# Kernel tuning notes

Hardware: AMD Instinct MI355X
Metric: run time of the kernel (lower is better)

Reference implementation:

```python
import jax, jax.numpy as jnp
import numpy as np

SIM_THRESHOLD = 0.65  # recall() returns decoded memory only if best_sim > 0.65
EPS = 1e-8            # torch F.cosine_similarity default eps


def setup_inputs() -> dict:
    key = jax.random.key(0)
    k1, k2, k3, k4 = jax.random.split(key, 4)
    dim, seq, n_mem = 1024, 2048, 131072
    bound = 1.0 / np.sqrt(dim)  # nn.Linear default init scale
    return {
        "query": jax.random.normal(k1, (seq, dim), dtype=jnp.float32),
        "bank": jax.random.normal(k2, (n_mem, dim), dtype=jnp.float32),
        "w_dec": jax.random.uniform(k3, (dim, dim), dtype=jnp.float32, minval=-bound, maxval=bound),
        "b_dec": jax.random.uniform(k4, (dim,), dtype=jnp.float32, minval=-bound, maxval=bound),
    }


def reference(query, bank, w_dec, b_dec):
    # q = query.detach().mean(dim=0)
    q = query.mean(axis=0)                                   # [dim]
    # cosine similarity of q against every stored memory (batched version of
    # the per-item F.cosine_similarity loop): dot / (max(||a||,eps)*max(||b||,eps))
    q_norm = jnp.maximum(jnp.linalg.norm(q), EPS)
    bank_norms = jnp.maximum(jnp.linalg.norm(bank, axis=1), EPS)  # [N]
    sims = (bank @ q) / (bank_norms * q_norm)                 # [N]
    idx = jnp.argmax(sims)
    best_sim = sims[idx]
    best_mem = bank[idx]                                      # [dim]
    # decoder(best.embedding): Linear(dim, dim)
    decoded = best_mem @ w_dec.T + b_dec                      # [dim]
    # original returns None below threshold; model as zeros to keep static shape
    return jnp.where(best_sim > SIM_THRESHOLD, decoded, jnp.zeros_like(decoded))
```

## Files before the change

### kernel.cpp

```cpp
#include <hip/hip_runtime.h>

#define EPS 1e-8f
#define THR 0.65f

constexpr int DIM  = 1024;
constexpr int SEQ  = 2048;
constexpr int NMEM = 131072;

constexpr int NCOPY    = 8;
constexpr int SIM_BLKS = 2048;
constexpr int ROWS_PER_WAVE = NMEM / (SIM_BLKS * 4);

typedef float f4 __attribute__((ext_vector_type(4)));

constexpr int WS_Q     = 8192;
constexpr int WS_QNORM = 9216;
constexpr int WS_BESTS = 9218;

__global__ void init_kernel(float* __restrict__ ws) {
    ((float4*)ws)[blockIdx.x * 256 + threadIdx.x] = make_float4(0.f, 0.f, 0.f, 0.f);
}

__global__ void qsum_kernel(const float* __restrict__ query, float* __restrict__ ws) {
    const float4* q4 = (const float4*)query;
    int tid = threadIdx.x;
    int r0  = blockIdx.x * 8;
    float4 s = make_float4(0.f, 0.f, 0.f, 0.f);
    #pragma unroll
    for (int r = 0; r < 8; ++r) {
        float4 v = q4[(size_t)(r0 + r) * 256 + tid];
        s.x += v.x; s.y += v.y; s.z += v.z; s.w += v.w;
    }
    float* dst = ws + (blockIdx.x & (NCOPY - 1)) * DIM + tid * 4;
    atomicAdd(dst + 0, s.x);
    atomicAdd(dst + 1, s.y);
    atomicAdd(dst + 2, s.z);
    atomicAdd(dst + 3, s.w);
}

__global__ void qfinal_kernel(float* __restrict__ ws) {
    __shared__ float red[4];
    int tid = threadIdx.x;
    float4 v = make_float4(0.f, 0.f, 0.f, 0.f);
    #pragma unroll
    for (int c = 0; c < NCOPY; ++c) {
        float4 p = ((float4*)ws)[c * 256 + tid];
        v.x += p.x; v.y += p.y; v.z += p.z; v.w += p.w;
    }
    const float inv = 1.0f / (float)SEQ;
    v.x *= inv; v.y *= inv; v.z *= inv; v.w *= inv;
    ((float4*)(ws + WS_Q))[tid] = v;
    float ss = v.x * v.x + v.y * v.y + v.z * v.z + v.w * v.w;
    #pragma unroll
    for (int m = 32; m >= 1; m >>= 1) ss += __shfl_xor(ss, m);
    int lane = tid & 63, wid = tid >> 6;
    if (lane == 0) red[wid] = ss;
    __syncthreads();
    if (tid == 0) {
        float tot = red[0] + red[1] + red[2] + red[3];
        ws[WS_QNORM] = fmaxf(sqrtf(tot), EPS);
    }
}

__device__ __forceinline__ unsigned int float_to_ordered(float f) {
    unsigned int b = __float_as_uint(f);
    return (b & 0x80000000u) ? ~b : (b | 0x80000000u);
}

__device__ __forceinline__ unsigned long long pack_best(float sim, int idx) {
    return ((unsigned long long)float_to_ordered(sim) << 32) |
           (unsigned int)(~(unsigned int)idx);
}

__launch_bounds__(256, 4)
__global__ void sim_kernel(const float* __restrict__ bank, const float* __restrict__ ws,
                           unsigned long long* __restrict__ bests) {
    __shared__ unsigned long long wbest[4];
    int tid  = threadIdx.x;
    int lane = tid & 63;
    int wid  = tid >> 6;

    const f4* q4 = (const f4*)(ws + WS_Q);
    f4 q0 = q4[lane +   0];
    f4 q1 = q4[lane +  64];
    f4 q2 = q4[lane + 128];
    f4 q3 = q4[lane + 192];
    float qn = ws[WS_QNORM];

    int gw   = blockIdx.x * 4 + wid;
    int row0 = gw * ROWS_PER_WAVE;

    float bestSim = -1e30f;
    int   bestIdx = 0;

    #pragma unroll
    for (int g = 0; g < ROWS_PER_WAVE / 4; ++g) {
        float dot[4], ss[4];
        f4 b[4][4];
        #pragma unroll
        for (int r = 0; r < 4; ++r) {
            const f4* bp = (const f4*)(bank + (size_t)(row0 + g * 4 + r) * DIM);
            b[r][0] = __builtin_nontemporal_load(bp + lane +   0);
            b[r][1] = __builtin_nontemporal_load(bp + lane +  64);
            b[r][2] = __builtin_nontemporal_load(bp + lane + 128);
            b[r][3] = __builtin_nontemporal_load(bp + lane + 192);
        }
        #pragma unroll
        for (int r = 0; r < 4; ++r) {
            dot[r] = b[r][0].x*q0.x + b[r][0].y*q0.y + b[r][0].z*q0.z + b[r][0].w*q0.w
                   + b[r][1].x*q1.x + b[r][1].y*q1.y + b[r][1].z*q1.z + b[r][1].w*q1.w
                   + b[r][2].x*q2.x + b[r][2].y*q2.y + b[r][2].z*q2.z + b[r][2].w*q2.w
                   + b[r][3].x*q3.x + b[r][3].y*q3.y + b[r][3].z*q3.z + b[r][3].w*q3.w;
            ss[r]  = b[r][0].x*b[r][0].x + b[r][0].y*b[r][0].y + b[r][0].z*b[r][0].z + b[r][0].w*b[r][0].w
                   + b[r][1].x*b[r][1].x + b[r][1].y*b[r][1].y + b[r][1].z*b[r][1].z + b[r][1].w*b[r][1].w
                   + b[r][2].x*b[r][2].x + b[r][2].y*b[r][2].y + b[r][2].z*b[r][2].z + b[r][2].w*b[r][2].w
                   + b[r][3].x*b[r][3].x + b[r][3].y*b[r][3].y + b[r][3].z*b[r][3].z + b[r][3].w*b[r][3].w;
        }
        #pragma unroll
        for (int m = 32; m >= 1; m >>= 1) {
            #pragma unroll
            for (int r = 0; r < 4; ++r) {
                dot[r] += __shfl_xor(dot[r], m);
                ss[r]  += __shfl_xor(ss[r], m);
            }
        }
        #pragma unroll
        for (int r = 0; r < 4; ++r) {
            float bn  = fmaxf(sqrtf(ss[r]), EPS);
            float sim = dot[r] / (bn * qn);
            if (sim > bestSim) { bestSim = sim; bestIdx = row0 + g * 4 + r; }
        }
    }

    if (lane == 0) wbest[wid] = pack_best(bestSim, bestIdx);
    __syncthreads();
    if (tid == 0) {
        unsigned long long p = wbest[0];
        if (wbest[1] > p) p = wbest[1];
        if (wbest[2] > p) p = wbest[2];
        if (wbest[3] > p) p = wbest[3];
        bests[blockIdx.x] = p;
    }
}

__global__ void decode_kernel(const float* __restrict__ bank,
                              const float* __restrict__ w_dec,
                              const float* __restrict__ b_dec,
                              const unsigned long long* __restrict__ bests,
                              float* __restrict__ out) {
    __shared__ unsigned long long red[256];
    __shared__ float mem[DIM];
    int tid = threadIdx.x;

    unsigned long long p = bests[tid];
    #pragma unroll
    for (int i = 1; i < SIM_BLKS / 256; ++i) {
        unsigned long long v = bests[tid + i * 256];
        if (v > p) p = v;
    }
    red[tid] = p;
    __syncthreads();
    #pragma unroll
    for (int s = 128; s >= 1; s >>= 1) {
        if (tid < s) {
            if (red[tid + s] > red[tid]) red[tid] = red[tid + s];
        }
        __syncthreads();
    }
    p = red[0];
    unsigned int u = (unsigned int)(p >> 32);
    unsigned int fb = (u & 0x80000000u) ? (u & 0x7FFFFFFFu) : ~u;
    float sim = __uint_as_float(fb);
    int idx   = (int)(~(unsigned int)(p & 0xFFFFFFFFu));

    ((float4*)mem)[tid] = ((const float4*)(bank + (size_t)idx * DIM))[tid];
    __syncthreads();

    bool ok  = sim > THR;
    int lane = tid & 63, wid = tid >> 6;
    int row  = blockIdx.x * 4 + wid;

    const float4* wp = (const float4*)(w_dec + (size_t)row * DIM);
    const float4* m4 = (const float4*)mem;
    float dot = 0.f;
    #pragma unroll
    for (int it = 0; it < 4; ++it) {
        float4 w = wp[lane + it * 64];
        float4 m = m4[lane + it * 64];
        dot += w.x * m.x + w.y * m.y + w.z * m.z + w.w * m.w;
    }
    #pragma unroll
    for (int m = 32; m >= 1; m >>= 1) dot += __shfl_xor(dot, m);

    if (lane == 0) out[row] = ok ? (dot + b_dec[row]) : 0.0f;
}

extern "C" void kernel_launch(void* const* d_in, const int* in_sizes, int n_in,
                              void* d_out, int out_size, void* d_ws, size_t ws_size,
                              hipStream_t stream) {
    const float* query = (const float*)d_in[0];
    const float* bank  = (const float*)d_in[1];
    const float* w_dec = (const float*)d_in[2];
    const float* b_dec = (const float*)d_in[3];
    float* out = (float*)d_out;
    float* ws  = (float*)d_ws;
    unsigned long long* bests = (unsigned long long*)(ws + WS_BESTS);

    init_kernel<<<NCOPY, 256, 0, stream>>>(ws);
    qsum_kernel<<<SEQ / 8, 256, 0, stream>>>(query, ws);
    qfinal_kernel<<<1, 256, 0, stream>>>(ws);
    sim_kernel<<<SIM_BLKS, 256, 0, stream>>>(bank, ws, bests);
    decode_kernel<<<256, 256, 0, stream>>>(bank, w_dec, b_dec, bests, out);
}
```

Baseline: 110.6 us.

## Replace atomic query-mean reduction with two-stage deterministic partial-sum kernels

The query column sum no longer uses float atomics into replicated buffers plus init and final kernels. A first kernel writes per-block partial sums to workspace, and a second kernel of 8 blocks reduces them, writing the mean and per-slice squared-norm partials. The sim kernel now combines those partials into the query norm itself. This removes one launch and the atomic contention, at the cost of an extra 1 MB of partial-sum traffic; the launch_bounds occupancy hint on sim_kernel is also relaxed.

```diff
diff --git a/kernel.cpp b/kernel.cpp
--- a/kernel.cpp
+++ b/kernel.cpp
@@ -7,58 +7,47 @@
 constexpr int SEQ  = 2048;
 constexpr int NMEM = 131072;
 
-constexpr int NCOPY    = 8;
 constexpr int SIM_BLKS = 2048;
 constexpr int ROWS_PER_WAVE = NMEM / (SIM_BLKS * 4);
 
 typedef float f4 __attribute__((ext_vector_type(4)));
 
-constexpr int WS_Q     = 8192;
-constexpr int WS_QNORM = 9216;
-constexpr int WS_BESTS = 9218;
-
-__global__ void init_kernel(float* __restrict__ ws) {
-    ((float4*)ws)[blockIdx.x * 256 + threadIdx.x] = make_float4(0.f, 0.f, 0.f, 0.f);
-}
-
-__global__ void qsum_kernel(const float* __restrict__ query, float* __restrict__ ws) {
-    const float4* q4 = (const float4*)query;
-    int tid = threadIdx.x;
-    int r0  = blockIdx.x * 8;
-    float4 s = make_float4(0.f, 0.f, 0.f, 0.f);
-    #pragma unroll
-    for (int r = 0; r < 8; ++r) {
-        float4 v = q4[(size_t)(r0 + r) * 256 + tid];
-        s.x += v.x; s.y += v.y; s.z += v.z; s.w += v.w;
-    }
-    float* dst = ws + (blockIdx.x & (NCOPY - 1)) * DIM + tid * 4;
-    atomicAdd(dst + 0, s.x);
-    atomicAdd(dst + 1, s.y);
-    atomicAdd(dst + 2, s.z);
-    atomicAdd(dst + 3, s.w);
-}
-
-__global__ void qfinal_kernel(float* __restrict__ ws) {
-    __shared__ float red[4];
-    int tid = threadIdx.x;
-    float4 v = make_float4(0.f, 0.f, 0.f, 0.f);
-    #pragma unroll
-    for (int c = 0; c < NCOPY; ++c) {
-        float4 p = ((float4*)ws)[c * 256 + tid];
-        v.x += p.x; v.y += p.y; v.z += p.z; v.w += p.w;
-    }
-    const float inv = 1.0f / (float)SEQ;
-    v.x *= inv; v.y *= inv; v.z *= inv; v.w *= inv;
-    ((float4*)(ws + WS_Q))[tid] = v;
-    float ss = v.x * v.x + v.y * v.y + v.z * v.z + v.w * v.w;
-    #pragma unroll
-    for (int m = 32; m >= 1; m >>= 1) ss += __shfl_xor(ss, m);
-    int lane = tid & 63, wid = tid >> 6;
-    if (lane == 0) red[wid] = ss;
-    __syncthreads();
-    if (tid == 0) {
-        float tot = red[0] + red[1] + red[2] + red[3];
-        ws[WS_QNORM] = fmaxf(sqrtf(tot), EPS);
+constexpr int WS_Q     = 262144;
+constexpr int WS_SSP   = 263168;
+constexpr int WS_BESTS = 263178;
+
+__global__ void qsumA_kernel(const float* __restrict__ query, float* __restrict__ ws) {
+    int t = threadIdx.x;
+    int b = blockIdx.x;
+    const f4* qp = (const f4*)(query + (size_t)b * 8 * DIM) + t;
+    f4 s = qp[0];
+    #pragma unroll
+    for (int r = 1; r < 8; ++r) s += qp[r * 256];
+    ((f4*)ws)[b * 256 + t] = s;
+}
+
+__global__ void qsumB_kernel(float* __restrict__ ws) {
+    __shared__ f4 lds[256];
+    int t = threadIdx.x;
+    int j = blockIdx.x;
+    int fc    = 32 * j + (t & 31);
+    int chunk = t >> 5;
+    const f4* pf = (const f4*)ws;
+    f4 s = pf[(32 * chunk) * 256 + fc];
+    #pragma unroll
+    for (int i = 1; i < 32; ++i) s += pf[(32 * chunk + i) * 256 + fc];
+    lds[t] = s;
+    __syncthreads();
+    if (t < 32) {
+        f4 f = lds[t];
+        #pragma unroll
+        for (int c = 1; c < 8; ++c) f += lds[t + 32 * c];
+        f *= (1.0f / (float)SEQ);
+        ((f4*)(ws + WS_Q))[32 * j + t] = f;
+        float ss = f.x * f.x + f.y * f.y + f.z * f.z + f.w * f.w;
+        #pragma unroll
+        for (int m = 16; m >= 1; m >>= 1) ss += __shfl_xor(ss, m);
+        if (t == 0) ws[WS_SSP + j] = ss;
     }
 }
 
@@ -72,7 +61,7 @@
            (unsigned int)(~(unsigned int)idx);
 }
 
-__launch_bounds__(256, 4)
+__launch_bounds__(256)
 __global__ void sim_kernel(const float* __restrict__ bank, const float* __restrict__ ws,
                            unsigned long long* __restrict__ bests) {
     __shared__ unsigned long long wbest[4];
@@ -80,12 +69,16 @@
     int lane = tid & 63;
     int wid  = tid >> 6;
 
+    float ssq = ws[WS_SSP + 0];
+    #pragma unroll
+    for (int j = 1; j < 8; ++j) ssq += ws[WS_SSP + j];
+    float qn = fmaxf(sqrtf(ssq), EPS);
+
     const f4* q4 = (const f4*)(ws + WS_Q);
     f4 q0 = q4[lane +   0];
     f4 q1 = q4[lane +  64];
     f4 q2 = q4[lane + 128];
     f4 q3 = q4[lane + 192];
-    float qn = ws[WS_QNORM];
 
     int gw   = blockIdx.x * 4 + wid;
     int row0 = gw * ROWS_PER_WAVE;
@@ -206,9 +199,8 @@
     float* ws  = (float*)d_ws;
     unsigned long long* bests = (unsigned long long*)(ws + WS_BESTS);
 
-    init_kernel<<<NCOPY, 256, 0, stream>>>(ws);
-    qsum_kernel<<<SEQ / 8, 256, 0, stream>>>(query, ws);
-    qfinal_kernel<<<1, 256, 0, stream>>>(ws);
+    qsumA_kernel<<<256, 256, 0, stream>>>(query, ws);
+    qsumB_kernel<<<8, 256, 0, stream>>>(ws);
     sim_kernel<<<SIM_BLKS, 256, 0, stream>>>(bank, ws, bests);
     decode_kernel<<<256, 256, 0, stream>>>(bank, w_dec, b_dec, bests, out);
 }
```

New measurement: 106.3 us. 3.9% less time.
